# Kernel tuning notes

Measured on AMD Instinct MI355X. Metric: run time of the kernel, lower is better.

Reference implementation:

```python
import jax, jax.numpy as jnp
import numpy as np

D_MODEL = 1024
NUM_HEADS = 16
HEAD_DIM = D_MODEL // NUM_HEADS


def setup_inputs() -> dict:
    key = jax.random.key(0)
    k_x, k_qkv, k_o = jax.random.split(key, 3)
    B, L = 2, 2048
    x = jax.random.normal(k_x, (B, L, D_MODEL), dtype=jnp.float32)
    # torch Linear weight [out, in]; y = x @ W.T. Scale ~ kaiming-uniform-ish.
    s = 1.0 / np.sqrt(D_MODEL)
    W_qkv = jax.random.uniform(k_qkv, (3 * D_MODEL, D_MODEL), dtype=jnp.float32, minval=-s, maxval=s)
    W_o = jax.random.uniform(k_o, (D_MODEL, D_MODEL), dtype=jnp.float32, minval=-s, maxval=s)
    return {"x": x, "W_qkv": W_qkv, "W_o": W_o}


def reference(x, W_qkv, W_o):
    B, L, D = x.shape
    H, dk = NUM_HEADS, HEAD_DIM
    qkv = (x @ W_qkv.T).reshape(B, L, 3, H, dk)
    q = qkv[:, :, 0].transpose(0, 2, 1, 3)  # [B,H,L,dk]
    k = qkv[:, :, 1].transpose(0, 2, 1, 3)
    v = qkv[:, :, 2].transpose(0, 2, 1, 3)
    scale = 1.0 / np.sqrt(dk).astype(np.float32)
    attn = jnp.einsum('bhqd,bhkd->bhqk', q, k) * scale  # [B,H,L,L]
    causal = jnp.tril(jnp.ones((L, L), dtype=bool))
    attn = jnp.where(causal, attn, -jnp.inf)
    attn = jax.nn.softmax(attn, axis=-1)
    y = jnp.einsum('bhqk,bhkd->bhqd', attn, v)  # [B,H,L,dk]
    y = y.transpose(0, 2, 1, 3).reshape(B, L, D)
    return y @ W_o.T
```

## Files before the change

### kernel.cpp

```cpp
#include <hip/hip_runtime.h>

typedef unsigned short u16;
typedef unsigned int   u32;

typedef __attribute__((ext_vector_type(4)))  float  f32x4;
typedef __attribute__((ext_vector_type(16))) float  f32x16;
typedef __attribute__((ext_vector_type(4)))  u32    u32x4;
typedef __attribute__((ext_vector_type(8)))  __bf16 bf16x8;

#define B_  2
#define L_  2048
#define H_  16

__device__ static inline u16 f2bf(float f) {
  u32 u = __builtin_bit_cast(u32, f);
  u32 r = u + 0x7fffu + ((u >> 16) & 1u);
  return (u16)(r >> 16);
}
__device__ static inline u32 pack2(float a, float b) {
  return (u32)f2bf(a) | ((u32)f2bf(b) << 16);
}
__device__ static inline u32 pack2t(float a, float b) {
  return __builtin_amdgcn_perm(__builtin_bit_cast(u32, b),
                               __builtin_bit_cast(u32, a), 0x07060302u);
}

__device__ static inline void swap32p(u32& a, u32& b) {
  auto r = __builtin_amdgcn_permlane32_swap(a, b, false, false);
  a = r[0]; b = r[1];
}

__device__ static inline void gload_lds16(const u16* g, u16* lds) {
  __builtin_amdgcn_global_load_lds((__attribute__((address_space(1))) void*)(g),
                                   (__attribute__((address_space(3))) void*)(lds),
                                   16, 0, 0);
}

__global__ __launch_bounds__(256) void cvt3_kernel(
    const float4* __restrict__ a, uint2* __restrict__ ao, int na,
    const float4* __restrict__ b, uint2* __restrict__ bo, int nb,
    const float4* __restrict__ c, uint2* __restrict__ co, int nc)
{
  const int step = gridDim.x * 256;
  constexpr int nq = 1024 * 1024 / 4;
  for (int i = blockIdx.x * 256 + threadIdx.x; i < na; i += step) {
    float4 f = a[i];
    ao[i] = make_uint2(pack2(f.x, f.y), pack2(f.z, f.w));
  }
  for (int i = blockIdx.x * 256 + threadIdx.x; i < nb; i += step) {
    float4 f = b[i];
    const float s = (i < nq) ? 0.125f : 1.0f;
    bo[i] = make_uint2(pack2(f.x * s, f.y * s), pack2(f.z * s, f.w * s));
  }
  for (int i = blockIdx.x * 256 + threadIdx.x; i < nc; i += step) {
    float4 f = c[i];
    co[i] = make_uint2(pack2(f.x, f.y), pack2(f.z, f.w));
  }
}

template <bool OUT_F32, int NT, bool DBUF>
__global__ __launch_bounds__(256) void gemm_bt_kernel(
    const u16* __restrict__ A, const u16* __restrict__ Bt, void* __restrict__ Cv,
    const int K, const int N)
{
  constexpr int NB = DBUF ? 2 : 1;
  constexpr int JT = NT / 32;
  __shared__ __attribute__((aligned(16))) u16 Al[NB][128 * 64];
  __shared__ __attribute__((aligned(16))) u16 Bl[NB][NT * 64];

  const int tid  = threadIdx.x;
  const int w    = tid >> 6;
  const int lane = tid & 63;
  const int m0 = blockIdx.y * 128;
  const int n0 = blockIdx.x * NT;
  const int mo = (w >> 1) * 64;
  const int no = (w & 1) * (NT / 2);

  const int sr8  = lane >> 3;
  const int scol = (((lane & 7) ^ ((lane >> 3) & 7)) * 8);

  const f32x4 zero = {0.f, 0.f, 0.f, 0.f};
  f32x4 acc[4][JT];
  #pragma unroll
  for (int i = 0; i < 4; ++i)
    #pragma unroll
    for (int j = 0; j < JT; ++j) acc[i][j] = zero;

  const int frow = lane & 15;
  const int fg   = lane >> 4;

  auto stage = [&](int buf, int k0) {
    #pragma unroll
    for (int inst = 0; inst < 4; ++inst) {
      const int r = w * 32 + inst * 8 + sr8;
      gload_lds16(A + (size_t)(m0 + r) * K + k0 + scol, &Al[buf][(w * 32 + inst * 8) * 64]);
    }
    #pragma unroll
    for (int inst = 0; inst < NT / 32; ++inst) {
      const int r = w * (NT / 4) + inst * 8 + sr8;
      gload_lds16(Bt + (size_t)(n0 + r) * K + k0 + scol, &Bl[buf][(w * (NT / 4) + inst * 8) * 64]);
    }
  };

  if (DBUF) stage(0, 0);

  int cur = 0;
  for (int k0 = 0; k0 < K; k0 += 64) {
    __syncthreads();
    if (DBUF) {
      if (k0 + 64 < K) stage(cur ^ 1, k0 + 64);
    } else {
      stage(0, k0);
      __syncthreads();
    }
    #pragma unroll
    for (int ks = 0; ks < 2; ++ks) {
      const int fco = ((ks * 4 + fg) ^ (frow & 7)) * 8;
      bf16x8 af[4], bfr[JT];
      #pragma unroll
      for (int i = 0; i < 4; ++i)
        af[i] = *(const bf16x8*)&Al[cur][(mo + i * 16 + frow) * 64 + fco];
      #pragma unroll
      for (int j = 0; j < JT; ++j)
        bfr[j] = *(const bf16x8*)&Bl[cur][(no + j * 16 + frow) * 64 + fco];
      #pragma unroll
      for (int i = 0; i < 4; ++i)
        #pragma unroll
        for (int j = 0; j < JT; ++j)
          acc[i][j] = __builtin_amdgcn_mfma_f32_16x16x32_bf16(af[i], bfr[j], acc[i][j], 0, 0, 0);
    }
    if (DBUF) cur ^= 1;
  }

  const int crow0 = m0 + mo + (lane >> 4) * 4;
  const int ccol0 = n0 + no + (lane & 15);
  #pragma unroll
  for (int i = 0; i < 4; ++i)
    #pragma unroll
    for (int j = 0; j < JT; ++j)
      #pragma unroll
      for (int r = 0; r < 4; ++r) {
        const size_t idx = (size_t)(crow0 + i * 16 + r) * N + (ccol0 + j * 16);
        if (OUT_F32) ((float*)Cv)[idx] = acc[i][j][r];
        else         ((u16*)Cv)[idx]   = f2bf(acc[i][j][r]);
      }
}

__global__ __launch_bounds__(256, 4) void attn_mfma_kernel(const u16* __restrict__ qkv,
                                                           u16* __restrict__ y)
{
  __shared__ __attribute__((aligned(16))) unsigned char smem[32768];

  const int tid  = threadIdx.x;
  const int w    = tid >> 6;
  const int lane = tid & 63;
  const int ql   = lane & 31;
  const int hi   = lane >> 5;
  const int qh   = w >> 1;
  const int kh   = w & 1;
  const int bh   = blockIdx.x;
  const int bb   = bh >> 4;
  const int hh   = bh & 15;
  const size_t rb = (size_t)bb * L_;

  const int a  = blockIdx.y & 7;
  const int cc = blockIdx.y >> 3;
  const int qt = (cc == 0) ? a : (cc == 1) ? (31 - a) : (cc == 2) ? (8 + a) : (23 - a);

  u16* Kt   = (u16*)(smem);
  u32* Vtd  = (u32*)(smem + 16384);
  float* Ocmb = (float*)smem;
  float* Lcmb = (float*)(smem + 16384);

  const int kkp = lane & 31;
  const int dc  = 2 * w + (lane >> 5);

  const int ksr = w * 16 + (lane >> 3);
  const int ksc = (((lane & 7) ^ ((lane >> 3) & 7)) * 8);

  const int q0 = qt * 64;
  const int qb = q0 + qh * 32;
  const int n  = qt + 1;

  bf16x8 qf[4];
  #pragma unroll
  for (int s = 0; s < 4; ++s)
    qf[s] = *(const bf16x8*)(qkv + (rb + qb + ql) * 3072 + hh * 64 + s * 16 + 8 * hi);

  f32x16 oacc0 = {}, oacc1 = {};
  float lsum = 0.f;

  auto stageK = [&](int buf, int kt) {
    #pragma unroll
    for (int inst = 0; inst < 2; ++inst)
      gload_lds16(qkv + (rb + kt + ksr + inst * 8) * 3072 + 1024 + hh * 64 + ksc,
                  &Kt[buf * 4096 + (w * 16 + inst * 8) * 64]);
  };
  auto loadV = [&](int kt, uint4& va, uint4& vb) {
    const u16* vp = qkv + (rb + kt + 2 * kkp) * 3072 + 2048 + hh * 64 + dc * 8;
    va = *(const uint4*)vp;
    vb = *(const uint4*)(vp + 3072);
  };
  auto writeV = [&](int buf, uint4 va, uint4 vb) {
    u16 a16[8], b16[8];
    *(uint4*)a16 = va; *(uint4*)b16 = vb;
    #pragma unroll
    for (int i = 0; i < 8; ++i)
      Vtd[buf * 2048 + (dc * 8 + i) * 32 + 4 * ((kkp >> 2) ^ i) + (kkp & 3)] =
          (u32)a16[i] | ((u32)b16[i] << 16);
  };

  {
    stageK(0, 0);
    uint4 va, vb;
    loadV(0, va, vb);
    writeV(0, va, vb);
  }

  int cur = 0;
  for (int it = 0; it < n; ++it) {
    __syncthreads();

    const int  kt       = it * 64;
    const bool havenext = (it + 1) < n;
    uint4 va, vb;
    if (havenext) {
      stageK(cur ^ 1, kt + 64);
      loadV(kt + 64, va, vb);
    }

    const bool diag = (kt == q0);
    if (!(diag && kh > qh)) {
      f32x16 sacc = {};
      __builtin_amdgcn_s_setprio(1);
      #pragma unroll
      for (int s = 0; s < 4; ++s) {
        bf16x8 kf = *(const bf16x8*)&Kt[cur * 4096 + (kh * 32 + ql) * 64 +
                                        (((2 * s + hi) ^ (ql & 7)) * 8)];
        sacc = __builtin_amdgcn_mfma_f32_32x32x16_bf16(kf, qf[s], sacc, 0, 0, 0);
      }
      __builtin_amdgcn_s_setprio(0);

      u32 u[8];
      if (diag && kh == qh) {
        #pragma unroll
        for (int j = 0; j < 8; ++j) {
          const int r0  = 2 * j;
          const int k0r = (r0 & 3) + 8 * (r0 >> 2) + 4 * hi;
          const float p0 = (k0r     > ql) ? 0.f : __expf(sacc[r0]);
          const float p1 = (k0r + 1 > ql) ? 0.f : __expf(sacc[r0 + 1]);
          lsum += p0 + p1;
          u[j] = pack2t(p0, p1);
        }
      } else {
        #pragma unroll
        for (int j = 0; j < 8; ++j) {
          const float p0 = __expf(sacc[2 * j]);
          const float p1 = __expf(sacc[2 * j + 1]);
          lsum += p0 + p1;
          u[j] = pack2t(p0, p1);
        }
      }

      swap32p(u[0], u[2]); swap32p(u[1], u[3]);
      swap32p(u[4], u[6]); swap32p(u[5], u[7]);
      const bf16x8 pf0 = __builtin_bit_cast(bf16x8, (u32x4){u[0], u[1], u[2], u[3]});
      const bf16x8 pf1 = __builtin_bit_cast(bf16x8, (u32x4){u[4], u[5], u[6], u[7]});

      __builtin_amdgcn_s_setprio(1);
      #pragma unroll
      for (int dt = 0; dt < 2; ++dt) {
        f32x16& oa = dt ? oacc1 : oacc0;
        const int d = dt * 32 + ql;
        bf16x8 vf0 = *(const bf16x8*)&Vtd[cur * 2048 + d * 32 + 4 * ((4 * kh + hi) ^ (ql & 7))];
        oa = __builtin_amdgcn_mfma_f32_32x32x16_bf16(vf0, pf0, oa, 0, 0, 0);
        bf16x8 vf1 = *(const bf16x8*)&Vtd[cur * 2048 + d * 32 + 4 * ((4 * kh + 2 + hi) ^ (ql & 7))];
        oa = __builtin_amdgcn_mfma_f32_32x32x16_bf16(vf1, pf1, oa, 0, 0, 0);
      }
      __builtin_amdgcn_s_setprio(0);
    }

    if (havenext) writeV(cur ^ 1, va, vb);
    cur ^= 1;
  }

  lsum += __shfl_xor(lsum, 32);

  __syncthreads();
  if (kh == 1) {
    #pragma unroll
    for (int dt = 0; dt < 2; ++dt)
      #pragma unroll
      for (int rq = 0; rq < 4; ++rq) {
        const f32x16& oa = dt ? oacc1 : oacc0;
        *(f32x4*)&Ocmb[(qh * 8 + dt * 4 + rq) * 256 + lane * 4] =
            (f32x4){oa[4 * rq], oa[4 * rq + 1], oa[4 * rq + 2], oa[4 * rq + 3]};
      }
    if (hi == 0) Lcmb[qh * 32 + ql] = lsum;
  }
  __syncthreads();
  if (kh == 0) {
    const float inv = 1.f / (lsum + Lcmb[qh * 32 + ql]);
    u16* yp = y + (rb + qb + ql) * 1024 + hh * 64;
    #pragma unroll
    for (int dt = 0; dt < 2; ++dt)
      #pragma unroll
      for (int rq = 0; rq < 4; ++rq) {
        const f32x16& oa = dt ? oacc1 : oacc0;
        const f32x4 oc = *(const f32x4*)&Ocmb[(qh * 8 + dt * 4 + rq) * 256 + lane * 4];
        const float v0 = (oa[4 * rq]     + oc[0]) * inv;
        const float v1 = (oa[4 * rq + 1] + oc[1]) * inv;
        const float v2 = (oa[4 * rq + 2] + oc[2]) * inv;
        const float v3 = (oa[4 * rq + 3] + oc[3]) * inv;
        *(uint2*)(yp + dt * 32 + 8 * rq + 4 * hi) = make_uint2(pack2(v0, v1), pack2(v2, v3));
      }
  }
}

extern "C" void kernel_launch(void* const* d_in, const int* in_sizes, int n_in,
                              void* d_out, int out_size, void* d_ws, size_t ws_size,
                              hipStream_t stream)
{
  const float* x    = (const float*)d_in[0];
  const float* Wqkv = (const float*)d_in[1];
  const float* Wo   = (const float*)d_in[2];
  float* out = (float*)d_out;

  u16* xb    = (u16*)d_ws;
  u16* Wqkvb = xb    + (size_t)4096 * 1024;
  u16* Wob   = Wqkvb + (size_t)3072 * 1024;
  u16* qkv   = Wob   + (size_t)1024 * 1024;
  u16* y     = qkv   + (size_t)4096 * 3072;

  cvt3_kernel<<<dim3(2048), dim3(256), 0, stream>>>(
      (const float4*)x,    (uint2*)xb,    4096 * 1024 / 4,
      (const float4*)Wqkv, (uint2*)Wqkvb, 3072 * 1024 / 4,
      (const float4*)Wo,   (uint2*)Wob,   1024 * 1024 / 4);

  gemm_bt_kernel<false, 128, false><<<dim3(3072 / 128, 4096 / 128), dim3(256), 0, stream>>>(
      xb, Wqkvb, qkv, 1024, 3072);
  attn_mfma_kernel<<<dim3(B_ * H_, 32), dim3(256), 0, stream>>>(qkv, y);
  gemm_bt_kernel<true, 64, true><<<dim3(1024 / 64, 4096 / 128), dim3(256), 0, stream>>>(
      y, Wob, out, 1024, 1024);
}
```

Baseline: 159.2 us.

## Replace QKV projection GEMM with 256x256-tile eight-wave pipelined kernel

```diff
diff --git a/kernel.cpp b/kernel.cpp
--- a/kernel.cpp
+++ b/kernel.cpp
@@ -144,6 +144,127 @@
         if (OUT_F32) ((float*)Cv)[idx] = acc[i][j][r];
         else         ((u16*)Cv)[idx]   = f2bf(acc[i][j][r]);
       }
+}
+
+__global__ __launch_bounds__(512, 2) void gemm256_kernel(
+    const u16* __restrict__ A, const u16* __restrict__ Bt, u16* __restrict__ C,
+    const int K, const int N)
+{
+  __shared__ __attribute__((aligned(16))) u16 Al[2][256 * 64];
+  __shared__ __attribute__((aligned(16))) u16 Bl[2][256 * 64];
+
+  const int tid  = threadIdx.x;
+  const int w    = tid >> 6;
+  const int lane = tid & 63;
+  const int wm   = w >> 2;
+  const int wn   = w & 3;
+  const int frow = lane & 15;
+  const int fg   = lane >> 4;
+  const int sr8  = lane >> 3;
+  const int scol = (((lane & 7) ^ ((lane >> 3) & 7)) * 8);
+
+  const int nbx = N >> 8;
+  int id = blockIdx.y * gridDim.x + blockIdx.x;
+  const int cpx = (gridDim.x * gridDim.y) >> 3;
+  id = (id & 7) * cpx + (id >> 3);
+  const int m0 = (id / nbx) * 256;
+  const int n0 = (id % nbx) * 256;
+
+  f32x4 acc[8][4];
+  #pragma unroll
+  for (int i = 0; i < 8; ++i)
+    #pragma unroll
+    for (int j = 0; j < 4; ++j) acc[i][j] = (f32x4){0.f, 0.f, 0.f, 0.f};
+
+  auto stageA = [&](int buf, int h, int k0) {
+    #pragma unroll
+    for (int j = 0; j < 2; ++j) {
+      const int rbase = h * 128 + w * 16 + j * 8;
+      gload_lds16(A + (size_t)(m0 + rbase + sr8) * K + k0 + scol, &Al[buf][rbase * 64]);
+    }
+  };
+  auto stageB = [&](int buf, int h, int k0) {
+    #pragma unroll
+    for (int j = 0; j < 2; ++j) {
+      const int rbase = h * 128 + w * 16 + j * 8;
+      gload_lds16(Bt + (size_t)(n0 + rbase + sr8) * K + k0 + scol, &Bl[buf][rbase * 64]);
+    }
+  };
+
+#define PHASE(CBUF, Q, STAGE_STMT)                                              \
+  {                                                                             \
+    constexpr int mq = (Q) >> 1, nq = (Q) & 1;                                  \
+    bf16x8 af[2][4];                                                            \
+    bf16x8 bfr[2][2];                                                           \
+    _Pragma("unroll")                                                           \
+    for (int ks = 0; ks < 2; ++ks) {                                            \
+      const int fco = ((ks * 4 + fg) ^ (frow & 7)) * 8;                         \
+      _Pragma("unroll")                                                         \
+      for (int i = 0; i < 4; ++i)                                               \
+        af[ks][i] = *(const bf16x8*)&Al[CBUF][(wm * 128 + mq * 64 + i * 16 + frow) * 64 + fco]; \
+      _Pragma("unroll")                                                         \
+      for (int j = 0; j < 2; ++j)                                               \
+        bfr[ks][j] = *(const bf16x8*)&Bl[CBUF][(wn * 64 + nq * 32 + j * 16 + frow) * 64 + fco]; \
+    }                                                                           \
+    STAGE_STMT;                                                                 \
+    __builtin_amdgcn_s_barrier();                                               \
+    asm volatile("s_waitcnt lgkmcnt(0)" ::: "memory");                          \
+    __builtin_amdgcn_sched_barrier(0);                                          \
+    __builtin_amdgcn_s_setprio(1);                                              \
+    _Pragma("unroll")                                                           \
+    for (int ks = 0; ks < 2; ++ks)                                              \
+      _Pragma("unroll")                                                         \
+      for (int i = 0; i < 4; ++i)                                               \
+        _Pragma("unroll")                                                       \
+        for (int j = 0; j < 2; ++j)                                             \
+          acc[mq * 4 + i][nq * 2 + j] = __builtin_amdgcn_mfma_f32_16x16x32_bf16(\
+              af[ks][i], bfr[ks][j], acc[mq * 4 + i][nq * 2 + j], 0, 0, 0);     \
+    __builtin_amdgcn_s_setprio(0);                                              \
+  }
+
+  const int KT = K >> 6;
+
+  stageA(0, 0, 0); stageA(0, 1, 0);
+  stageB(0, 0, 0); stageB(0, 1, 0);
+  if (KT > 1) {
+    stageA(1, 0, 64);
+    asm volatile("s_waitcnt vmcnt(2)" ::: "memory");
+  } else {
+    asm volatile("s_waitcnt vmcnt(0)" ::: "memory");
+  }
+  __builtin_amdgcn_s_barrier();
+
+  for (int t = 0; t < KT; ++t) {
+    const int  c  = t & 1;
+    const bool h1 = (t + 1) < KT;
+    const int  kn = (t + 1) << 6;
+
+    PHASE(c, 0, if (h1) stageA(c ^ 1, 1, kn));
+    __builtin_amdgcn_s_barrier();
+    PHASE(c, 1, if (h1) stageB(c ^ 1, 0, kn));
+    __builtin_amdgcn_s_barrier();
+    PHASE(c, 2, if (h1) stageB(c ^ 1, 1, kn));
+    __builtin_amdgcn_s_barrier();
+    PHASE(c, 3, );
+    if (t + 2 < KT) {
+      stageA(c, 0, (t + 2) << 6);
+      asm volatile("s_waitcnt vmcnt(2)" ::: "memory");
+    } else {
+      asm volatile("s_waitcnt vmcnt(0)" ::: "memory");
+    }
+    __builtin_amdgcn_s_barrier();
+  }
+#undef PHASE
+
+  const int crow0 = m0 + wm * 128 + fg * 4;
+  const int ccol0 = n0 + wn * 64 + frow;
+  #pragma unroll
+  for (int i = 0; i < 8; ++i)
+    #pragma unroll
+    for (int j = 0; j < 4; ++j)
+      #pragma unroll
+      for (int r = 0; r < 4; ++r)
+        C[(size_t)(crow0 + i * 16 + r) * N + (ccol0 + j * 16)] = f2bf(acc[i][j][r]);
 }
 
 __global__ __launch_bounds__(256, 4) void attn_mfma_kernel(const u16* __restrict__ qkv,
@@ -337,7 +458,7 @@
       (const float4*)Wqkv, (uint2*)Wqkvb, 3072 * 1024 / 4,
       (const float4*)Wo,   (uint2*)Wob,   1024 * 1024 / 4);
 
-  gemm_bt_kernel<false, 128, false><<<dim3(3072 / 128, 4096 / 128), dim3(256), 0, stream>>>(
+  gemm256_kernel<<<dim3(3072 / 256, 4096 / 256), dim3(512), 0, stream>>>(
       xb, Wqkvb, qkv, 1024, 3072);
   attn_mfma_kernel<<<dim3(B_ * H_, 32), dim3(256), 0, stream>>>(qkv, y);
   gemm_bt_kernel<true, 64, true><<<dim3(1024 / 64, 4096 / 128), dim3(256), 0, stream>>>(
```

New measurement: 167.3 us. 1.05x slower.
